# Kernel tuning notes

Hardware: AMD Instinct MI355X
Metric: run time of the kernel (lower is better)

The kernel has to match this reference:

```python
import jax, jax.numpy as jnp
import numpy as np

NUM_HEADS = 16
HEAD_SIZE = 64
EMB = NUM_HEADS * HEAD_SIZE
B, S = 2, 2048


def setup_inputs() -> dict:
    key = jax.random.key(0)
    ks = jax.random.split(key, 8)
    return {
        "values": jax.random.normal(ks[0], (B, S, EMB), dtype=jnp.float32),
        "keys": jax.random.normal(ks[1], (B, S, EMB), dtype=jnp.float32),
        "queries": jax.random.normal(ks[2], (B, S, EMB), dtype=jnp.float32),
        "mask": jnp.ones((B, 1, 1, S), dtype=jnp.int32),
        "Wq": jax.random.normal(ks[3], (HEAD_SIZE, HEAD_SIZE), dtype=jnp.float32) / np.sqrt(HEAD_SIZE),
        "Wk": jax.random.normal(ks[4], (HEAD_SIZE, HEAD_SIZE), dtype=jnp.float32) / np.sqrt(HEAD_SIZE),
        "Wv": jax.random.normal(ks[5], (HEAD_SIZE, HEAD_SIZE), dtype=jnp.float32) / np.sqrt(HEAD_SIZE),
        "Wout": jax.random.normal(ks[6], (EMB, EMB), dtype=jnp.float32) / np.sqrt(EMB),
        "bout": jax.random.normal(ks[7], (EMB,), dtype=jnp.float32) * 0.01,
    }


def reference(values, keys, queries, mask, Wq, Wk, Wv, Wout, bout):
    n, q_len, E = queries.shape
    H, D = NUM_HEADS, HEAD_SIZE
    # split heads: [n, len, H, D]
    v = values.reshape(n, -1, H, D)
    k = keys.reshape(n, -1, H, D)
    q = queries.reshape(n, q_len, H, D)
    # per-head shared linears (torch Linear: x @ W.T), no bias
    v = jnp.einsum("nkhd,cd->nkhc", v, Wv)
    k = jnp.einsum("nkhd,cd->nkhc", k, Wk)
    q = jnp.einsum("nqhd,cd->nqhc", q, Wq)
    # scores: [n, H, q, k]
    energy = jnp.einsum("nqhd,nkhd->nhqk", q, k)
    energy = jnp.where(mask == 0, jnp.float32(-1e28), energy)
    # NOTE: source scales by sqrt(embedding_size), not head_size
    attn = jax.nn.softmax(energy / jnp.sqrt(jnp.float32(E)), axis=3)
    out = jnp.einsum("nhqk,nkhd->nqhd", attn, v).reshape(n, q_len, E)
    return out @ Wout.T + bout
```

## Files before the change

### kernel.cpp

```cpp
#include <hip/hip_runtime.h>
#include <hip/hip_bf16.h>


#define NHB 16
#define HS  64
#define EMB 1024
#define BB  2
#define SS  2048
#define NT  (SS / 64)

typedef __bf16 bf16_t;
typedef bf16_t bf16x8 __attribute__((ext_vector_type(8)));
typedef bf16_t bf16x4 __attribute__((ext_vector_type(4)));
typedef float  f32x4  __attribute__((ext_vector_type(4)));

__device__ __forceinline__ f32x4 mfma16(bf16x8 a, bf16x8 b, f32x4 c) {
    return __builtin_amdgcn_mfma_f32_16x16x32_bf16(a, b, c, 0, 0, 0);
}

__device__ __forceinline__ float fast_exp2(float x) {
#if __has_builtin(__builtin_amdgcn_exp2f)
    return __builtin_amdgcn_exp2f(x);
#else
    float r;
    asm("v_exp_f32 %0, %1" : "=v"(r) : "v"(x));
    return r;
#endif
}

__device__ __forceinline__ bf16x8 cvt8f(float4 x, float4 y) {
    bf16x8 r;
    r[0] = (bf16_t)x.x; r[1] = (bf16_t)x.y; r[2] = (bf16_t)x.z; r[3] = (bf16_t)x.w;
    r[4] = (bf16_t)y.x; r[5] = (bf16_t)y.y; r[6] = (bf16_t)y.z; r[7] = (bf16_t)y.w;
    return r;
}

__global__ __launch_bounds__(512, 4) void proj_kernel(
    const float* __restrict__ queries, const float* __restrict__ keys,
    const float* __restrict__ values,
    const float* __restrict__ Wq, const float* __restrict__ Wk,
    const float* __restrict__ Wv,
    bf16_t* __restrict__ Qb, bf16_t* __restrict__ Kb, bf16_t* __restrict__ Vt)
{
    __shared__ bf16_t Ws[3][64][72];

    const int tid  = threadIdx.x;
    const int wave = tid >> 6, lane = tid & 63;
    const int q4 = lane >> 4, l16 = lane & 15;
    const int s0 = blockIdx.x * 128;
    const int h  = blockIdx.y, n = blockIdx.z;

    #pragma unroll
    for (int i = 0; i < 6; ++i) {
        int g = i * 512 + tid;
        int mW = g >> 10;
        int idx4 = g & 1023;
        const float* wp = (mW == 0) ? Wq : (mW == 1) ? Wk : Wv;
        float4 v = ((const float4*)wp)[idx4];
        int r = idx4 >> 4, c = (idx4 & 15) * 4;
        Ws[mW][r][c+0] = (bf16_t)v.x; Ws[mW][r][c+1] = (bf16_t)v.y;
        Ws[mW][r][c+2] = (bf16_t)v.z; Ws[mW][r][c+3] = (bf16_t)v.w;
    }

    const size_t xrow = (size_t)(n * SS + s0 + wave * 16 + l16) * EMB + h * HS;
    const float* xsrc[3] = {queries, keys, values};
    bf16x8 xb[3][2];
    #pragma unroll
    for (int p = 0; p < 3; ++p) {
        const float* rp = xsrc[p] + xrow;
        float4 t0 = *(const float4*)(rp + q4 * 8);
        float4 t1 = *(const float4*)(rp + q4 * 8 + 4);
        float4 t2 = *(const float4*)(rp + 32 + q4 * 8);
        float4 t3 = *(const float4*)(rp + 32 + q4 * 8 + 4);
        xb[p][0] = cvt8f(t0, t1);
        xb[p][1] = cvt8f(t2, t3);
    }

    __syncthreads();

    const size_t headBase = (size_t)(n * NHB + h) * SS * HS;

    #pragma unroll
    for (int p = 0; p < 3; ++p) {
        bf16x8 wf[4][2];
        #pragma unroll
        for (int ct = 0; ct < 4; ++ct)
            #pragma unroll
            for (int kk = 0; kk < 2; ++kk)
                wf[ct][kk] = *(const bf16x8*)&Ws[p][ct * 16 + l16][kk * 32 + q4 * 8];

        if (p < 2) {
            bf16_t* dst = (p == 0) ? Qb : Kb;
            const float sc = (p == 0) ? (0.03125f * 1.44269504f) : 1.0f;
            bf16x8 lo, hi;
            #pragma unroll
            for (int ct = 0; ct < 4; ++ct) {
                f32x4 acc = {};
                acc = mfma16(wf[ct][0], xb[p][0], acc);
                acc = mfma16(wf[ct][1], xb[p][1], acc);
                #pragma unroll
                for (int i = 0; i < 4; ++i) {
                    bf16_t v = (bf16_t)(acc[i] * sc);
                    if (ct < 2) lo[ct * 4 + i] = v;
                    else        hi[(ct - 2) * 4 + i] = v;
                }
            }
            bf16_t* rp = dst + headBase
                + (size_t)(s0 + wave * 16 + l16) * HS + q4 * 16;
            *(bf16x8*)rp = lo;
            *(bf16x8*)(rp + 8) = hi;
        } else {
            #pragma unroll
            for (int ct = 0; ct < 4; ++ct) {
                f32x4 acc = {};
                acc = mfma16(xb[2][0], wf[ct][0], acc);
                acc = mfma16(xb[2][1], wf[ct][1], acc);
                bf16x4 pk;
                #pragma unroll
                for (int i = 0; i < 4; ++i) pk[i] = (bf16_t)acc[i];
                *(bf16x4*)&Vt[headBase + (size_t)(ct * 16 + l16) * SS
                              + s0 + (wave >> 1) * 32 + q4 * 8 + (wave & 1) * 4] = pk;
            }
        }
    }
}

__global__ __launch_bounds__(512) void attn_kernel(
    const bf16_t* __restrict__ Qb, const bf16_t* __restrict__ Kb,
    const bf16_t* __restrict__ Vt, const int* __restrict__ mask,
    bf16_t* __restrict__ Og)
{
    __shared__ __align__(16) unsigned char smem[37376];
    auto Ks = (bf16_t(*)[64][72])(smem);
    auto Vs = (bf16_t(*)[64][72])(smem + 18432);
    auto Ms = (float(*)[64])(smem + 36864);
    float* fbuf = (float*)smem;
    float* lbuf = (float*)(smem + 32768);

    const int tid = threadIdx.x;
    const int w = tid >> 6, lane = tid & 63;
    const int q4 = lane >> 4, l16 = lane & 15;
    const int wq = w & 3, wk = w >> 2;
    const int qt = blockIdx.x, h = blockIdx.y, n = blockIdx.z;
    const size_t headBase = (size_t)(n * NHB + h) * SS * HS;
    const int* mrow = mask + n * SS;

    const int sr = tid >> 3, sc = (tid & 7) * 8;
    const bf16_t* kb_src = Kb + headBase + (size_t)sr * HS + sc;
    const bf16_t* vt_src = Vt + headBase + (size_t)sr * SS + sc;

    bf16x8 bq[2][2];
    #pragma unroll
    for (int st = 0; st < 2; ++st) {
        const bf16_t* qptr = Qb + headBase
            + (size_t)(qt * 128 + wq * 32 + st * 16 + l16) * HS;
        bq[st][0] = *(const bf16x8*)&qptr[q4 * 8];
        bq[st][1] = *(const bf16x8*)&qptr[32 + q4 * 8];
    }

    bf16x8 ones;
    #pragma unroll
    for (int i = 0; i < 8; ++i) ones[i] = (bf16_t)1.0f;

    f32x4 oaccT[2][4] = {};
    f32x4 lacc[2] = {};

    *(bf16x8*)&Ks[0][sr][sc] = *(const bf16x8*)kb_src;
    *(bf16x8*)&Vs[0][sr][sc] = *(const bf16x8*)vt_src;
    if (tid < 64) Ms[0][tid] = mrow[tid] ? 0.0f : -3e38f;
    __syncthreads();

    for (int kt = 0; kt < NT; ++kt) {
        const int cur = kt & 1;
        const bool has_next = (kt + 1) < NT;
        bf16x8 gk, gv; float gm = 0.f;
        if (has_next) {
            const int k0n = (kt + 1) * 64;
            gk = *(const bf16x8*)(kb_src + (size_t)k0n * HS);
            gv = *(const bf16x8*)(vt_src + k0n);
            if (tid < 64) gm = mrow[k0n + tid] ? 0.0f : -3e38f;
        }

        f32x4 sacc[2][2];
        #pragma unroll
        for (int c2 = 0; c2 < 2; ++c2) {
            const int ct = wk * 2 + c2;
            float4 bias = *(const float4*)&Ms[cur][ct * 16 + q4 * 4];
            f32x4 b4 = {bias.x, bias.y, bias.z, bias.w};
            sacc[0][c2] = b4; sacc[1][c2] = b4;
            bf16x8 ak0 = *(const bf16x8*)&Ks[cur][ct * 16 + l16][q4 * 8];
            bf16x8 ak1 = *(const bf16x8*)&Ks[cur][ct * 16 + l16][32 + q4 * 8];
            #pragma unroll
            for (int st = 0; st < 2; ++st) {
                sacc[st][c2] = mfma16(ak0, bq[st][0], sacc[st][c2]);
                sacc[st][c2] = mfma16(ak1, bq[st][1], sacc[st][c2]);
            }
        }

        bf16x4 pv[2][2];
        #pragma unroll
        for (int c2 = 0; c2 < 2; ++c2)
            #pragma unroll
            for (int st = 0; st < 2; ++st) {
                bf16x4 pk;
                #pragma unroll
                for (int j = 0; j < 4; ++j)
                    pk[j] = (bf16_t)fast_exp2(sacc[st][c2][j]);
                pv[st][c2] = pk;
            }

        bf16x8 pa[2];
        #pragma unroll
        for (int st = 0; st < 2; ++st)
            pa[st] = __builtin_shufflevector(pv[st][0], pv[st][1],
                                             0, 1, 2, 3, 4, 5, 6, 7);
        #pragma unroll
        for (int dt = 0; dt < 4; ++dt) {
            bf16x8 av = *(const bf16x8*)&Vs[cur][dt * 16 + l16][wk * 32 + q4 * 8];
            oaccT[0][dt] = mfma16(av, pa[0], oaccT[0][dt]);
            oaccT[1][dt] = mfma16(av, pa[1], oaccT[1][dt]);
        }
        lacc[0] = mfma16(ones, pa[0], lacc[0]);
        lacc[1] = mfma16(ones, pa[1], lacc[1]);

        if (has_next) {
            const int nxt = 1 - cur;
            *(bf16x8*)&Ks[nxt][sr][sc] = gk;
            *(bf16x8*)&Vs[nxt][sr][sc] = gv;
            if (tid < 64) Ms[nxt][tid] = gm;
        }
        __syncthreads();
    }

    float ls[2] = {lacc[0][0], lacc[1][0]};

    if (w >= 4) {
        const int lanecol = wq * 64 + lane;
        #pragma unroll
        for (int st = 0; st < 2; ++st) {
            #pragma unroll
            for (int dt = 0; dt < 4; ++dt)
                #pragma unroll
                for (int j = 0; j < 4; ++j)
                    fbuf[(st * 16 + dt * 4 + j) * 256 + lanecol] = oaccT[st][dt][j];
            lbuf[st * 256 + lanecol] = ls[st];
        }
    }
    __syncthreads();
    if (w < 4) {
        const int lanecol = wq * 64 + lane;
        #pragma unroll
        for (int st = 0; st < 2; ++st) {
            #pragma unroll
            for (int dt = 0; dt < 4; ++dt)
                #pragma unroll
                for (int j = 0; j < 4; ++j)
                    oaccT[st][dt][j] += fbuf[(st * 16 + dt * 4 + j) * 256 + lanecol];
            ls[st] += lbuf[st * 256 + lanecol];
        }
        #pragma unroll
        for (int st = 0; st < 2; ++st) {
            const float inv = 1.f / ls[st];
            const int qrow = qt * 128 + wq * 32 + st * 16 + l16;
            bf16_t* obase = Og + ((size_t)(n * SS + qrow)) * EMB + h * HS;
            #pragma unroll
            for (int dt = 0; dt < 4; ++dt) {
                bf16x4 ov;
                #pragma unroll
                for (int j = 0; j < 4; ++j) ov[j] = (bf16_t)(oaccT[st][dt][j] * inv);
                *(bf16x4*)&obase[dt * 16 + q4 * 4] = ov;
            }
        }
    }
}

__global__ __launch_bounds__(256) void wcvt_kernel(
    const float* __restrict__ W, bf16_t* __restrict__ Wb)
{
    const int idx = blockIdx.x * 256 + threadIdx.x;
    float4 a = ((const float4*)W)[idx * 2];
    float4 b = ((const float4*)W)[idx * 2 + 1];
    *(bf16x8*)&Wb[idx * 8] = cvt8f(a, b);
}

__global__ __launch_bounds__(512) void outproj_kernel(
    const bf16_t* __restrict__ Og, const bf16_t* __restrict__ Wb,
    const float* __restrict__ bout, float* __restrict__ out)
{
    __shared__ bf16_t As[2][128][40];
    __shared__ bf16_t Bs[2][128][40];

    const int tid = threadIdx.x;
    const int w = tid >> 6, lane = tid & 63;
    const int q4 = lane >> 4, l16 = lane & 15;
    const int wr = w >> 2, wc = w & 3;
    const int t0 = blockIdx.x * 128, c0 = blockIdx.y * 128;

    const int sr = tid >> 2, sc = (tid & 3) * 8;
    const bf16_t* asrc = Og + (size_t)(t0 + sr) * EMB + sc;
    const bf16_t* bsrc = Wb + (size_t)(c0 + sr) * EMB + sc;

    f32x4 acc[4][2] = {};

    *(bf16x8*)&As[0][sr][sc] = *(const bf16x8*)asrc;
    *(bf16x8*)&Bs[0][sr][sc] = *(const bf16x8*)bsrc;
    __syncthreads();

    const int NE = EMB / 32;
    for (int et = 0; et < NE; ++et) {
        const int cur = et & 1;
        const bool has_next = (et + 1) < NE;
        bf16x8 ga, gb;
        if (has_next) {
            const int e0 = (et + 1) * 32;
            ga = *(const bf16x8*)(asrc + e0);
            gb = *(const bf16x8*)(bsrc + e0);
        }

        bf16x8 af[4], bfr[2];
        #pragma unroll
        for (int st = 0; st < 4; ++st)
            af[st] = *(const bf16x8*)&As[cur][wr * 64 + st * 16 + l16][q4 * 8];
        #pragma unroll
        for (int ct = 0; ct < 2; ++ct)
            bfr[ct] = *(const bf16x8*)&Bs[cur][wc * 32 + ct * 16 + l16][q4 * 8];
        #pragma unroll
        for (int st = 0; st < 4; ++st)
            #pragma unroll
            for (int ct = 0; ct < 2; ++ct)
                acc[st][ct] = mfma16(bfr[ct], af[st], acc[st][ct]);

        if (has_next) {
            const int nxt = 1 - cur;
            *(bf16x8*)&As[nxt][sr][sc] = ga;
            *(bf16x8*)&Bs[nxt][sr][sc] = gb;
        }
        __syncthreads();
    }

    #pragma unroll
    for (int st = 0; st < 4; ++st) {
        const int t = t0 + wr * 64 + st * 16 + l16;
        float* orow = out + (size_t)t * EMB + c0 + wc * 32;
        #pragma unroll
        for (int ct = 0; ct < 2; ++ct) {
            const float4 bb = *(const float4*)&bout[c0 + wc * 32 + ct * 16 + q4 * 4];
            float4 v = {acc[st][ct][0] + bb.x, acc[st][ct][1] + bb.y,
                        acc[st][ct][2] + bb.z, acc[st][ct][3] + bb.w};
            *(float4*)&orow[ct * 16 + q4 * 4] = v;
        }
    }
}

extern "C" void kernel_launch(void* const* d_in, const int* in_sizes, int n_in,
                              void* d_out, int out_size, void* d_ws, size_t ws_size,
                              hipStream_t stream)
{
    const float* values  = (const float*)d_in[0];
    const float* keys    = (const float*)d_in[1];
    const float* queries = (const float*)d_in[2];
    const int*   mask    = (const int*)d_in[3];
    const float* Wq      = (const float*)d_in[4];
    const float* Wk      = (const float*)d_in[5];
    const float* Wv      = (const float*)d_in[6];
    const float* Wout    = (const float*)d_in[7];
    const float* bout    = (const float*)d_in[8];
    float* out = (float*)d_out;

    const size_t M8 = 8ull * 1024 * 1024;
    bf16_t* Qb = (bf16_t*)d_ws;
    bf16_t* Kb = (bf16_t*)((char*)d_ws + 1 * M8);
    bf16_t* Vt = (bf16_t*)((char*)d_ws + 2 * M8);
    bf16_t* Og = (bf16_t*)((char*)d_ws + 3 * M8);
    bf16_t* Wb = (bf16_t*)d_ws;

    proj_kernel<<<dim3(SS / 128, NHB, BB), 512, 0, stream>>>(
        queries, keys, values, Wq, Wk, Wv, Qb, Kb, Vt);
    attn_kernel<<<dim3(SS / 128, NHB, BB), 512, 0, stream>>>(
        Qb, Kb, Vt, mask, Og);
    wcvt_kernel<<<dim3(512), 256, 0, stream>>>(Wout, Wb);
    outproj_kernel<<<dim3((BB * SS) / 128, EMB / 128), 512, 0, stream>>>(
        Og, Wb, bout, out);
}
```

Measured before the change: 175.7 us.

## Fuse Wout conversion into outproj, shrink tiles, swizzle attention blocks across XCDs

Removes the separate Wout fp32-to-bf16 conversion kernel; the output projection now reads fp32 Wout and converts each tile in registers before staging it in LDS. The output projection tiles shrink from 128x128 to 64x64 with 256 threads, giving four times as many blocks to fill the CUs. The projection kernel also drops to 64-row, 256-thread blocks. The attention grid is flattened and remapped so that blocks on the same XCD (bid&7) work on the same heads, which is meant to improve L2 reuse of K and V. The trade-off is that fp32 Wout is re-read and re-converted by every row block, and smaller tiles reuse less data from LDS.

```diff
diff --git a/kernel.cpp b/kernel.cpp
--- a/kernel.cpp
+++ b/kernel.cpp
@@ -35,7 +35,7 @@
     return r;
 }
 
-__global__ __launch_bounds__(512, 4) void proj_kernel(
+__global__ __launch_bounds__(256, 4) void proj_kernel(
     const float* __restrict__ queries, const float* __restrict__ keys,
     const float* __restrict__ values,
     const float* __restrict__ Wq, const float* __restrict__ Wk,
@@ -47,12 +47,12 @@
     const int tid  = threadIdx.x;
     const int wave = tid >> 6, lane = tid & 63;
     const int q4 = lane >> 4, l16 = lane & 15;
-    const int s0 = blockIdx.x * 128;
+    const int s0 = blockIdx.x * 64;
     const int h  = blockIdx.y, n = blockIdx.z;
 
     #pragma unroll
-    for (int i = 0; i < 6; ++i) {
-        int g = i * 512 + tid;
+    for (int i = 0; i < 12; ++i) {
+        int g = i * 256 + tid;
         int mW = g >> 10;
         int idx4 = g & 1023;
         const float* wp = (mW == 0) ? Wq : (mW == 1) ? Wk : Wv;
@@ -141,7 +141,13 @@
     const int w = tid >> 6, lane = tid & 63;
     const int q4 = lane >> 4, l16 = lane & 15;
     const int wq = w & 3, wk = w >> 2;
-    const int qt = blockIdx.x, h = blockIdx.y, n = blockIdx.z;
+
+    const int bid = blockIdx.x;
+    const int r = bid & 7, t = bid >> 3;
+    const int gi = t >> 4, qt = t & 15;
+    const int g = gi * 8 + r;
+    const int h = g & 15, n = g >> 4;
+
     const size_t headBase = (size_t)(n * NHB + h) * SS * HS;
     const int* mrow = mask + n * SS;
 
@@ -274,73 +280,65 @@
     }
 }
 
-__global__ __launch_bounds__(256) void wcvt_kernel(
-    const float* __restrict__ W, bf16_t* __restrict__ Wb)
-{
-    const int idx = blockIdx.x * 256 + threadIdx.x;
-    float4 a = ((const float4*)W)[idx * 2];
-    float4 b = ((const float4*)W)[idx * 2 + 1];
-    *(bf16x8*)&Wb[idx * 8] = cvt8f(a, b);
-}
-
-__global__ __launch_bounds__(512) void outproj_kernel(
-    const bf16_t* __restrict__ Og, const bf16_t* __restrict__ Wb,
+__global__ __launch_bounds__(256, 4) void outproj_kernel(
+    const bf16_t* __restrict__ Og, const float* __restrict__ Wout,
     const float* __restrict__ bout, float* __restrict__ out)
 {
-    __shared__ bf16_t As[2][128][40];
-    __shared__ bf16_t Bs[2][128][40];
+    __shared__ bf16_t As[2][64][40];
+    __shared__ bf16_t Bs[2][64][40];
 
     const int tid = threadIdx.x;
     const int w = tid >> 6, lane = tid & 63;
     const int q4 = lane >> 4, l16 = lane & 15;
-    const int wr = w >> 2, wc = w & 3;
-    const int t0 = blockIdx.x * 128, c0 = blockIdx.y * 128;
-
-    const int sr = tid >> 2, sc = (tid & 3) * 8;
-    const bf16_t* asrc = Og + (size_t)(t0 + sr) * EMB + sc;
-    const bf16_t* bsrc = Wb + (size_t)(c0 + sr) * EMB + sc;
-
-    f32x4 acc[4][2] = {};
-
-    *(bf16x8*)&As[0][sr][sc] = *(const bf16x8*)asrc;
-    *(bf16x8*)&Bs[0][sr][sc] = *(const bf16x8*)bsrc;
+    const int wr = w >> 1, wc = w & 1;
+    const int t0 = blockIdx.x * 64, c0 = blockIdx.y * 64;
+
+    const int ar = tid >> 2, ac = (tid & 3) * 8;
+    const bf16_t* asrc = Og + (size_t)(t0 + ar) * EMB + ac;
+    const float*  bsrc = Wout + (size_t)(c0 + ar) * EMB + ac;
+
+    f32x4 acc[2][2] = {};
+
+    *(bf16x8*)&As[0][ar][ac] = *(const bf16x8*)asrc;
+    *(bf16x8*)&Bs[0][ar][ac] = cvt8f(*(const float4*)bsrc, *(const float4*)(bsrc + 4));
     __syncthreads();
 
     const int NE = EMB / 32;
     for (int et = 0; et < NE; ++et) {
         const int cur = et & 1;
         const bool has_next = (et + 1) < NE;
-        bf16x8 ga, gb;
+        bf16x8 ga; float4 gb0, gb1;
         if (has_next) {
             const int e0 = (et + 1) * 32;
-            ga = *(const bf16x8*)(asrc + e0);
-            gb = *(const bf16x8*)(bsrc + e0);
-        }
-
-        bf16x8 af[4], bfr[2];
-        #pragma unroll
-        for (int st = 0; st < 4; ++st)
-            af[st] = *(const bf16x8*)&As[cur][wr * 64 + st * 16 + l16][q4 * 8];
+            ga  = *(const bf16x8*)(asrc + e0);
+            gb0 = *(const float4*)(bsrc + e0);
+            gb1 = *(const float4*)(bsrc + e0 + 4);
+        }
+
+        bf16x8 af[2], bfr[2];
+        #pragma unroll
+        for (int st = 0; st < 2; ++st)
+            af[st] = *(const bf16x8*)&As[cur][wr * 32 + st * 16 + l16][q4 * 8];
         #pragma unroll
         for (int ct = 0; ct < 2; ++ct)
             bfr[ct] = *(const bf16x8*)&Bs[cur][wc * 32 + ct * 16 + l16][q4 * 8];
         #pragma unroll
-        for (int st = 0; st < 4; ++st)
+        for (int st = 0; st < 2; ++st)
             #pragma unroll
             for (int ct = 0; ct < 2; ++ct)
                 acc[st][ct] = mfma16(bfr[ct], af[st], acc[st][ct]);
 
         if (has_next) {
             const int nxt = 1 - cur;
-            *(bf16x8*)&As[nxt][sr][sc] = ga;
-            *(bf16x8*)&Bs[nxt][sr][sc] = gb;
+            *(bf16x8*)&As[nxt][ar][ac] = ga;
+            *(bf16x8*)&Bs[nxt][ar][ac] = cvt8f(gb0, gb1);
         }
         __syncthreads();
     }
 
     #pragma unroll
-    for (int st = 0; st < 4; ++st) {
-        const int t = t0 + wr * 64 + st * 16 + l16;
+    for (int st = 0; st < 2; ++st) {
+        const int t = t0 + wr * 32 + st * 16 + l16;
         float* orow = out + (size_t)t * EMB + c0 + wc * 32;
         #pragma unroll
         for (int ct = 0; ct < 2; ++ct) {
@@ -372,13 +370,11 @@
     bf16_t* Kb = (bf16_t*)((char*)d_ws + 1 * M8);
     bf16_t* Vt = (bf16_t*)((char*)d_ws + 2 * M8);
     bf16_t* Og = (bf16_t*)((char*)d_ws + 3 * M8);
-    bf16_t* Wb = (bf16_t*)d_ws;
-
-    proj_kernel<<<dim3(SS / 128, NHB, BB), 512, 0, stream>>>(
+
+    proj_kernel<<<dim3(SS / 64, NHB, BB), 256, 0, stream>>>(
         queries, keys, values, Wq, Wk, Wv, Qb, Kb, Vt);
-    attn_kernel<<<dim3(SS / 128, NHB, BB), 512, 0, stream>>>(
+    attn_kernel<<<dim3(512), 512, 0, stream>>>(
         Qb, Kb, Vt, mask, Og);
-    wcvt_kernel<<<dim3(512), 256, 0, stream>>>(Wout, Wb);
-    outproj_kernel<<<dim3((BB * SS) / 128, EMB / 128), 512, 0, stream>>>(
-        Og, Wb, bout, out);
-}
+    outproj_kernel<<<dim3((BB * SS) / 64, EMB / 64), 256, 0, stream>>>(
+        Og, Wout, bout, out);
+}
```

Result: no change. 172.6 us (-1.8%).
